# Optimization experiments

Hardware: AMD Instinct MI355X
Metric: run time of the kernel (lower is better)

Reference implementation:

```python
import jax, jax.numpy as jnp
import numpy as np

B, L, D, H, DK, DV = 2, 2048, 1024, 16, 64, 64


def setup_inputs() -> dict:
    key = jax.random.key(0)
    ks = jax.random.split(key, 9)
    s = 0.02
    q = jax.random.normal(ks[0], (B, L, D), dtype=jnp.float32)
    k = jax.random.normal(ks[1], (B, L, D), dtype=jnp.float32)
    v = jax.random.normal(ks[2], (B, L, D), dtype=jnp.float32)
    # causal mask: mask==0 positions are masked out (matches masked_fill(mask==0, -1e9))
    mask = jnp.broadcast_to(jnp.tril(jnp.ones((L, L), dtype=jnp.int32)), (B, L, L))
    Wq = jax.random.normal(ks[3], (D, H * DK), dtype=jnp.float32) * s
    Wk = jax.random.normal(ks[4], (D, H * DK), dtype=jnp.float32) * s
    Wv = jax.random.normal(ks[5], (D, H * DV), dtype=jnp.float32) * s
    Wfc = jax.random.normal(ks[6], (H * DV, D), dtype=jnp.float32) * s
    gamma = jnp.ones((D,), dtype=jnp.float32)
    beta = jnp.zeros((D,), dtype=jnp.float32)
    return {"q": q, "k": k, "v": v, "Wq": Wq, "Wk": Wk, "Wv": Wv,
            "Wfc": Wfc, "gamma": gamma, "beta": beta, "mask": mask}


def reference(q, k, v, Wq, Wk, Wv, Wfc, gamma, beta, mask):
    residual = q
    # project and split heads: [B, H, L, dk]
    qh = (q @ Wq).reshape(B, L, H, DK).transpose(0, 2, 1, 3)
    kh = (k @ Wk).reshape(B, L, H, DK).transpose(0, 2, 1, 3)
    vh = (v @ Wv).reshape(B, L, H, DV).transpose(0, 2, 1, 3)
    temperature = jnp.asarray(DK, jnp.float32) ** 0.5
    scores = jnp.einsum('bhqd,bhkd->bhqk', qh / temperature, kh)  # [B,H,L,L]
    scores = jnp.where(mask[:, None, :, :] == 0, jnp.float32(-1e9), scores)
    attn = jax.nn.softmax(scores, axis=-1)  # dropout = identity (eval)
    out = jnp.einsum('bhqk,bhkd->bhqd', attn, vh)
    out = out.transpose(0, 2, 1, 3).reshape(B, L, H * DV)
    out = out @ Wfc + residual  # dropout = identity (eval)
    # LayerNorm, eps=1e-6
    mu = jnp.mean(out, axis=-1, keepdims=True)
    var = jnp.mean((out - mu) ** 2, axis=-1, keepdims=True)
    out = (out - mu) * jax.lax.rsqrt(var + 1e-6) * gamma + beta
    return out, attn
```

## Files before the change

kernel.cpp:

```cpp
#include <hip/hip_runtime.h>
#include <hip/hip_bf16.h>

#define NB 2
#define NL 2048
#define ND 1024
#define NH 16
#define NDK 64

typedef float fx4 __attribute__((ext_vector_type(4)));
typedef short sx8 __attribute__((ext_vector_type(8)));
typedef short sx4 __attribute__((ext_vector_type(4)));

static __device__ __forceinline__ short f2bf(float x) {
  __hip_bfloat16 h = __float2bfloat16(x);
  short s;
  __builtin_memcpy(&s, &h, 2);
  return s;
}

static __device__ __forceinline__ float ex2(float x) {
  float r; asm("v_exp_f32 %0, %1" : "=v"(r) : "v"(x)); return r;
}

__global__ __launch_bounds__(256) void wt_kernel(
    const float* __restrict__ Wq, const float* __restrict__ Wk,
    const float* __restrict__ Wv, const float* __restrict__ Wfc,
    short* __restrict__ wt)
{
  const float* W = (blockIdx.z==0)?Wq:(blockIdx.z==1)?Wk:(blockIdx.z==2)?Wv:Wfc;
  float sc = (blockIdx.z==0) ? 0.18033688011112042f : 1.0f;
  short* out = wt + (size_t)blockIdx.z*1024*1024;
  int n0 = blockIdx.x*64, k0 = blockIdx.y*64;
  __shared__ float t[64][65];
  int tid = threadIdx.x;
  int kr = tid>>2, ns = (tid&3)*16;
  #pragma unroll
  for (int i=0;i<4;i++){
    fx4 v = *(const fx4*)(W + (size_t)(k0+kr)*1024 + n0 + ns + i*4);
    t[kr][ns+i*4+0]=v[0]; t[kr][ns+i*4+1]=v[1];
    t[kr][ns+i*4+2]=v[2]; t[kr][ns+i*4+3]=v[3];
  }
  __syncthreads();
  int nr = tid>>2, ks = (tid&3)*16;
  sx8 o0,o1;
  #pragma unroll
  for (int i=0;i<8;i++){ o0[i]=f2bf(t[ks+i][nr]*sc); o1[i]=f2bf(t[ks+8+i][nr]*sc); }
  *(sx8*)(out + (size_t)(n0+nr)*1024 + k0 + ks)     = o0;
  *(sx8*)(out + (size_t)(n0+nr)*1024 + k0 + ks + 8) = o1;
}

__global__ __launch_bounds__(256) void cast_kernel(
    const float* __restrict__ q, const float* __restrict__ k,
    const float* __restrict__ v, short* __restrict__ qb,
    short* __restrict__ kb, short* __restrict__ vb)
{
  const float* src = (blockIdx.y==0)?q:(blockIdx.y==1)?k:v;
  short* dst = (blockIdx.y==0)?qb:(blockIdx.y==1)?kb:vb;
  size_t base = ((size_t)blockIdx.x*256 + threadIdx.x)*8;
  fx4 a = *(const fx4*)(src+base), b = *(const fx4*)(src+base+4);
  sx8 o;
  o[0]=f2bf(a[0]); o[1]=f2bf(a[1]); o[2]=f2bf(a[2]); o[3]=f2bf(a[3]);
  o[4]=f2bf(b[0]); o[5]=f2bf(b[1]); o[6]=f2bf(b[2]); o[7]=f2bf(b[3]);
  *(sx8*)(dst+base) = o;
}

__global__ __launch_bounds__(256) void gemm_kernel(
    const short* __restrict__ qb, const short* __restrict__ kb,
    const short* __restrict__ vb, const short* __restrict__ ao,
    const float* __restrict__ q, const short* __restrict__ wt,
    short* __restrict__ qh, short* __restrict__ kh, short* __restrict__ vtb,
    float* __restrict__ preln, int mode_base)
{
  int mode = mode_base + blockIdx.z;
  const short* Ab = (mode==0)?qb:(mode==1)?kb:(mode==2)?vb:ao;
  const short* Bw = wt + (size_t)mode*1048576;
  int m0 = blockIdx.y*128, n0 = blockIdx.x*128;
  __shared__ short Al[128*64];
  __shared__ short Bl[128*64];
  int tid = threadIdx.x;
  int w = tid>>6, l = tid&63, lr = l>>4, lc = l&15;
  int wm = w>>1, wn = w&1;
  int grow = l>>3, gcol = (l&7)*8;

  fx4 acc[4][4];
  #pragma unroll
  for (int i=0;i<4;i++)
    #pragma unroll
    for (int j=0;j<4;j++) acc[i][j] = (fx4)0.0f;

  for (int kb2=0; kb2<1024; kb2+=64) {
    #pragma unroll
    for (int p=0;p<4;p++){
      int rb = w*32 + p*8;
      __builtin_amdgcn_global_load_lds(
        (const __attribute__((address_space(1))) int*)(Ab + (size_t)(m0+rb+grow)*1024 + kb2 + gcol),
        (__attribute__((address_space(3))) int*)&Al[rb*64], 16, 0, 0);
      __builtin_amdgcn_global_load_lds(
        (const __attribute__((address_space(1))) int*)(Bw + (size_t)(n0+rb+grow)*1024 + kb2 + gcol),
        (__attribute__((address_space(3))) int*)&Bl[rb*64], 16, 0, 0);
    }
    __syncthreads();
    #pragma unroll
    for (int kk=0;kk<2;kk++){
      sx8 af[4], bfr[4];
      int oct = kk*4 + lr;
      #pragma unroll
      for (int i=0;i<4;i++){
        af[i]  = *(const sx8*)&Al[(wm*64 + i*16 + lc)*64 + oct*8];
        bfr[i] = *(const sx8*)&Bl[(wn*64 + i*16 + lc)*64 + oct*8];
      }
      #pragma unroll
      for (int i=0;i<4;i++)
        #pragma unroll
        for (int j=0;j<4;j++)
          acc[i][j] = __builtin_amdgcn_mfma_f32_16x16x32_bf16(af[i], bfr[j], acc[i][j], 0,0,0);
    }
    __syncthreads();
  }

  #pragma unroll
  for (int i=0;i<4;i++){
    int mrow0 = m0 + wm*64 + i*16 + lr*4;
    #pragma unroll
    for (int j=0;j<4;j++){
      int n = n0 + wn*64 + j*16 + lc;
      if (mode<=1) {
        short* dst = (mode==0)?qh:kh;
        int hh = n>>6, d = n&63;
        #pragma unroll
        for (int r=0;r<4;r++){
          int mr = mrow0 + r; int bb = mr>>11, lp = mr&2047;
          dst[((size_t)(bb*16+hh)*2048 + lp)*64 + d] = f2bf(acc[i][j][r]);
        }
      } else if (mode==2) {
        int hh = n>>6, d = n&63;
        int bb = mrow0>>11, lp = mrow0&2047;
        sx4 pv;
        #pragma unroll
        for (int r=0;r<4;r++) pv[r] = f2bf(acc[i][j][r]);
        *(sx4*)&vtb[((size_t)(bb*16+hh)*64 + d)*2048 + lp] = pv;
      } else {
        #pragma unroll
        for (int r=0;r<4;r++){
          int mr = mrow0 + r;
          preln[(size_t)mr*1024 + n] = acc[i][j][r] + q[(size_t)mr*1024 + n];
        }
      }
    }
  }
}

__global__ __launch_bounds__(256) void attn_kernel(
    const short* __restrict__ qh, const short* __restrict__ kh,
    const short* __restrict__ vt, short* __restrict__ ao,
    float* __restrict__ attn)
{
  int qt = 31 - (int)blockIdx.x;
  int bh = blockIdx.y;
  int qbase = qt*64;
  int tid = threadIdx.x, w = tid>>6, l = tid&63, lr = l>>4, lc = l&15;
  int qrow0 = qbase + w*16;
  int qrow_l = qrow0 + lc;
  int kend = qrow0 + 16;
  int knlim = (w + 2) & ~1;

  float* arow = attn + (size_t)bh*NL*NL;
  const short* qhb = qh + (size_t)bh*NL*64;
  const short* khb = kh + (size_t)bh*NL*64;
  const short* vtb = vt + (size_t)bh*64*NL;

  sx8 Qf0 = *(const sx8*)&qhb[(size_t)qrow_l*64 + lr*8];
  sx8 Qf1 = *(const sx8*)&qhb[(size_t)qrow_l*64 + 32 + lr*8];

  __shared__ short Kl[2][64][64];
  __shared__ short Vl[2][64][64];
  __shared__ short pl[4][16][40];

  int idx0 = w*64 + l;
  int idx1 = 256 + w*64 + l;
  int rA = idx0>>3, oA = idx0&7, rB = idx1>>3, oB = idx1&7;
  int ntile = qt + 1;

  {
    sx8 ka = *(const sx8*)&khb[(size_t)rA*64 + oA*8];
    sx8 kb = *(const sx8*)&khb[(size_t)rB*64 + oB*8];
    *(sx8*)&Kl[0][rA][(oA^(rA&7))*8] = ka;
    *(sx8*)&Kl[0][rB][(oB^(rB&7))*8] = kb;
  }
  __syncthreads();

  float ls = 0.0f;
  int buf = 0;
  #pragma unroll 1
  for (int t=0; t<ntile; t++){
    bool have_next = (t+1) < ntile;
    sx8 ka, kb;
    if (have_next){
      int nb = (t+1)*64;
      ka = *(const sx8*)&khb[(size_t)(nb+rA)*64 + oA*8];
      kb = *(const sx8*)&khb[(size_t)(nb+rB)*64 + oB*8];
    }
    bool diag = (t == qt);
    #pragma unroll
    for (int kn=0; kn<4; kn++){
      if (diag && kn > w) continue;
      int rk = kn*16 + lc;
      sx8 k0 = *(const sx8*)&Kl[buf][rk][((lr  ^(rk&7))*8)];
      sx8 k1 = *(const sx8*)&Kl[buf][rk][(((lr+4)^(rk&7))*8)];
      fx4 s = (fx4)0.0f;
      s = __builtin_amdgcn_mfma_f32_16x16x32_bf16(k0, Qf0, s, 0,0,0);
      s = __builtin_amdgcn_mfma_f32_16x16x32_bf16(k1, Qf1, s, 0,0,0);
      if (!diag || kn < w) {
        ls += (ex2(s[0]) + ex2(s[1])) + (ex2(s[2]) + ex2(s[3]));
      } else {
        int key0 = t*64 + kn*16 + lr*4;
        #pragma unroll
        for (int r=0;r<4;r++)
          ls += (key0 + r <= qrow_l) ? ex2(s[r]) : 0.0f;
      }
    }
    if (have_next){
      int nbuf = buf ^ 1;
      *(sx8*)&Kl[nbuf][rA][(oA^(rA&7))*8] = ka;
      *(sx8*)&Kl[nbuf][rB][(oB^(rB&7))*8] = kb;
    }
    __syncthreads();
    buf ^= 1;
  }
  ls += __shfl_xor(ls, 16, 64);
  ls += __shfl_xor(ls, 32, 64);
  float inv = 1.0f / ls;

  {
    int fs = ((kend + 31) >> 5) << 5;
    fx4 z = (fx4)0.0f;
    #pragma unroll 1
    for (int r=0; r<16; r++){
      float* rp = &arow[(size_t)(qrow0+r)*NL];
      for (int c = fs + l*4; c < NL; c += 256)
        __builtin_nontemporal_store(z, (fx4*)&rp[c]);
    }
  }

  {
    sx8 ka = *(const sx8*)&khb[(size_t)rA*64 + oA*8];
    sx8 kb = *(const sx8*)&khb[(size_t)rB*64 + oB*8];
    sx8 va = *(const sx8*)&vtb[(size_t)rA*NL + oA*8];
    sx8 vb = *(const sx8*)&vtb[(size_t)rB*NL + oB*8];
    *(sx8*)&Kl[0][rA][(oA^(rA&7))*8] = ka;
    *(sx8*)&Kl[0][rB][(oB^(rB&7))*8] = kb;
    *(sx8*)&Vl[0][rA][(oA^(rA&7))*8] = va;
    *(sx8*)&Vl[0][rB][(oB^(rB&7))*8] = vb;
  }
  __syncthreads();

  fx4 O[4];
  #pragma unroll
  for (int n=0;n<4;n++) O[n] = (fx4)0.0f;

  buf = 0;
  #pragma unroll 1
  for (int t=0; t<ntile; t++){
    int tb = t*64;
    bool have_next = (t+1) < ntile;
    sx8 ka, kb, va, vb;
    if (have_next){
      int nb = tb + 64;
      ka = *(const sx8*)&khb[(size_t)(nb+rA)*64 + oA*8];
      kb = *(const sx8*)&khb[(size_t)(nb+rB)*64 + oB*8];
      va = *(const sx8*)&vtb[(size_t)rA*NL + nb + oA*8];
      vb = *(const sx8*)&vtb[(size_t)rB*NL + nb + oB*8];
    }
    bool diag = (t == qt);
    #pragma unroll
    for (int kn=0; kn<4; kn++){
      fx4 p;
      if (!diag || kn <= w) {
        int rk = kn*16 + lc;
        sx8 k0 = *(const sx8*)&Kl[buf][rk][((lr  ^(rk&7))*8)];
        sx8 k1 = *(const sx8*)&Kl[buf][rk][(((lr+4)^(rk&7))*8)];
        fx4 s = (fx4)0.0f;
        s = __builtin_amdgcn_mfma_f32_16x16x32_bf16(k0, Qf0, s, 0,0,0);
        s = __builtin_amdgcn_mfma_f32_16x16x32_bf16(k1, Qf1, s, 0,0,0);
        if (!diag || kn < w) {
          #pragma unroll
          for (int r=0;r<4;r++) p[r] = ex2(s[r]) * inv;
        } else {
          int key0 = tb + kn*16 + lr*4;
          #pragma unroll
          for (int r=0;r<4;r++)
            p[r] = (key0 + r <= qrow_l) ? ex2(s[r]) * inv : 0.0f;
        }
      } else {
        p = (fx4)0.0f;
      }
      if (!diag || kn < knlim)
        __builtin_nontemporal_store(p, (fx4*)&arow[(size_t)qrow_l*NL + tb + kn*16 + lr*4]);
      sx4 pbv;
      #pragma unroll
      for (int r=0;r<4;r++) pbv[r] = f2bf(p[r]);
      *(sx4*)&pl[w][lc][(kn&1)*16 + lr*4] = pbv;
      if (kn & 1){
        sx8 pf = *(const sx8*)&pl[w][lc][lr*8];
        int t2 = kn>>1;
        #pragma unroll
        for (int n=0;n<4;n++){
          int rv = n*16 + lc;
          sx8 vf = *(const sx8*)&Vl[buf][rv][(((t2*4+lr)^(rv&7))*8)];
          O[n] = __builtin_amdgcn_mfma_f32_16x16x32_bf16(pf, vf, O[n], 0,0,0);
        }
      }
    }
    if (have_next){
      int nbuf = buf ^ 1;
      *(sx8*)&Kl[nbuf][rA][(oA^(rA&7))*8] = ka;
      *(sx8*)&Kl[nbuf][rB][(oB^(rB&7))*8] = kb;
      *(sx8*)&Vl[nbuf][rA][(oA^(rA&7))*8] = va;
      *(sx8*)&Vl[nbuf][rB][(oB^(rB&7))*8] = vb;
    }
    __syncthreads();
    buf ^= 1;
  }

  int bb = bh>>4, hh = bh&15;
  #pragma unroll
  for (int n=0;n<4;n++)
    #pragma unroll
    for (int r=0;r<4;r++)
      ao[((size_t)bb*NL + qrow0 + lr*4 + r)*1024 + hh*64 + n*16 + lc] = f2bf(O[n][r]);
}

__global__ __launch_bounds__(256) void ln_kernel(
    const float* __restrict__ preln, const float* __restrict__ gamma,
    const float* __restrict__ beta, float* __restrict__ out)
{
  int row = blockIdx.x, tid = threadIdx.x;
  fx4 x = *(const fx4*)&preln[(size_t)row*1024 + tid*4];
  float s  = x[0]+x[1]+x[2]+x[3];
  float sq = x[0]*x[0]+x[1]*x[1]+x[2]*x[2]+x[3]*x[3];
  #pragma unroll
  for (int off=1; off<64; off<<=1){
    s  += __shfl_xor(s,  off, 64);
    sq += __shfl_xor(sq, off, 64);
  }
  __shared__ float rs[4], rq[4];
  int w = tid>>6, l = tid&63;
  if (l==0){ rs[w]=s; rq[w]=sq; }
  __syncthreads();
  s  = rs[0]+rs[1]+rs[2]+rs[3];
  sq = rq[0]+rq[1]+rq[2]+rq[3];
  float mean = s*(1.0f/1024.0f);
  float var  = sq*(1.0f/1024.0f) - mean*mean;
  float rstd = rsqrtf(var + 1e-6f);
  fx4 g = *(const fx4*)&gamma[tid*4];
  fx4 b = *(const fx4*)&beta[tid*4];
  fx4 y;
  #pragma unroll
  for (int i=0;i<4;i++) y[i] = (x[i]-mean)*rstd*g[i] + b[i];
  *(fx4*)&out[(size_t)row*1024 + tid*4] = y;
}

extern "C" void kernel_launch(void* const* d_in, const int* in_sizes, int n_in,
                              void* d_out, int out_size, void* d_ws, size_t ws_size,
                              hipStream_t stream) {
  const float* q    = (const float*)d_in[0];
  const float* k    = (const float*)d_in[1];
  const float* v    = (const float*)d_in[2];
  const float* Wq   = (const float*)d_in[3];
  const float* Wk   = (const float*)d_in[4];
  const float* Wv   = (const float*)d_in[5];
  const float* Wfc  = (const float*)d_in[6];
  const float* gamma= (const float*)d_in[7];
  const float* beta = (const float*)d_in[8];

  float* out  = (float*)d_out;
  float* attn = out + (size_t)NB*NL*ND;

  char* ws = (char*)d_ws;
  short* wt    = (short*)(ws);
  short* qb    = (short*)(ws + ((size_t) 8<<20));
  short* kb    = (short*)(ws + ((size_t)16<<20));
  short* vb    = (short*)(ws + ((size_t)24<<20));
  short* qh    = (short*)(ws + ((size_t)32<<20));
  short* kh    = (short*)(ws + ((size_t)40<<20));
  short* vtb   = (short*)(ws + ((size_t)48<<20));
  short* ao    = (short*)(ws + ((size_t)56<<20));
  float* preln = (float*)(ws + ((size_t) 8<<20));

  wt_kernel<<<dim3(16,16,4), 256, 0, stream>>>(Wq, Wk, Wv, Wfc, wt);
  cast_kernel<<<dim3(2048,3), 256, 0, stream>>>(q, k, v, qb, kb, vb);
  gemm_kernel<<<dim3(8,32,3), 256, 0, stream>>>(qb,kb,vb,ao, q, wt, qh,kh,vtb, preln, 0);
  attn_kernel<<<dim3(32,32), 256, 0, stream>>>(qh, kh, vtb, ao, attn);
  gemm_kernel<<<dim3(8,32,1), 256, 0, stream>>>(qb,kb,vb,ao, q, wt, qh,kh,vtb, preln, 3);
  ln_kernel<<<4096, 256, 0, stream>>>(preln, gamma, beta, out);
}
```

Before: 284.1 us.

## Load K/V fragments directly from global into registers, dropping LDS staging and barriers

The attention kernel stops staging K and V tiles through double-buffered shared memory with block-wide barriers. Each wave now loads its MFMA operand fragments straight from global memory into registers, ping-ponging between two register sets for prefetch. This removes the LDS writes and reads and the __syncthreads per tile. In exchange, every wave loads the same K/V data separately (four times the global/L2 traffic), uses more registers, and issues V loads inside the tile without prefetch.

```diff
diff --git a/kernel.cpp b/kernel.cpp
--- a/kernel.cpp
+++ b/kernel.cpp
@@ -163,6 +163,7 @@
   int qrow_l = qrow0 + lc;
   int kend = qrow0 + 16;
   int knlim = (w + 2) & ~1;
+  int ntile = qt + 1;
 
   float* arow = attn + (size_t)bh*NL*NL;
   const short* qhb = qh + (size_t)bh*NL*64;
@@ -172,64 +173,101 @@
   sx8 Qf0 = *(const sx8*)&qhb[(size_t)qrow_l*64 + lr*8];
   sx8 Qf1 = *(const sx8*)&qhb[(size_t)qrow_l*64 + 32 + lr*8];
 
-  __shared__ short Kl[2][64][64];
-  __shared__ short Vl[2][64][64];
   __shared__ short pl[4][16][40];
 
-  int idx0 = w*64 + l;
-  int idx1 = 256 + w*64 + l;
-  int rA = idx0>>3, oA = idx0&7, rB = idx1>>3, oB = idx1&7;
-  int ntile = qt + 1;
-
-  {
-    sx8 ka = *(const sx8*)&khb[(size_t)rA*64 + oA*8];
-    sx8 kb = *(const sx8*)&khb[(size_t)rB*64 + oB*8];
-    *(sx8*)&Kl[0][rA][(oA^(rA&7))*8] = ka;
-    *(sx8*)&Kl[0][rB][(oB^(rB&7))*8] = kb;
-  }
-  __syncthreads();
-
   float ls = 0.0f;
-  int buf = 0;
+  float inv = 0.0f;
+  fx4 O[4];
+  #pragma unroll
+  for (int n=0;n<4;n++) O[n] = (fx4)0.0f;
+
+  auto loadK = [&](sx8 (&Kd)[8], int t){
+    int tb = t*64;
+    #pragma unroll
+    for (int kn=0;kn<4;kn++){
+      Kd[kn*2+0] = *(const sx8*)&khb[(size_t)(tb+kn*16+lc)*64 + lr*8];
+      Kd[kn*2+1] = *(const sx8*)&khb[(size_t)(tb+kn*16+lc)*64 + 32 + lr*8];
+    }
+  };
+
+  auto sumTile = [&](sx8 (&K)[8], int t){
+    bool diag = (t==qt);
+    int tb = t*64;
+    #pragma unroll
+    for (int kn=0;kn<4;kn++){
+      if (diag && kn>w) continue;
+      fx4 s = (fx4)0.0f;
+      s = __builtin_amdgcn_mfma_f32_16x16x32_bf16(K[kn*2+0], Qf0, s, 0,0,0);
+      s = __builtin_amdgcn_mfma_f32_16x16x32_bf16(K[kn*2+1], Qf1, s, 0,0,0);
+      if (!diag || kn<w){
+        ls += (ex2(s[0])+ex2(s[1])) + (ex2(s[2])+ex2(s[3]));
+      } else {
+        int key0 = tb + kn*16 + lr*4;
+        #pragma unroll
+        for (int r=0;r<4;r++)
+          ls += (key0+r <= qrow_l) ? ex2(s[r]) : 0.0f;
+      }
+    }
+  };
+
+  auto pvTile = [&](sx8 (&K)[8], int t){
+    int tb = t*64;
+    bool diag = (t==qt);
+    sx8 Vv[8];
+    #pragma unroll
+    for (int t2=0;t2<2;t2++)
+      #pragma unroll
+      for (int n=0;n<4;n++)
+        Vv[t2*4+n] = *(const sx8*)&vtb[(size_t)(n*16+lc)*NL + tb + t2*32 + lr*8];
+    #pragma unroll
+    for (int kn=0;kn<4;kn++){
+      fx4 p;
+      if (!diag || kn<=w){
+        fx4 s = (fx4)0.0f;
+        s = __builtin_amdgcn_mfma_f32_16x16x32_bf16(K[kn*2+0], Qf0, s, 0,0,0);
+        s = __builtin_amdgcn_mfma_f32_16x16x32_bf16(K[kn*2+1], Qf1, s, 0,0,0);
+        if (!diag || kn<w){
+          #pragma unroll
+          for (int r=0;r<4;r++) p[r] = ex2(s[r]) * inv;
+        } else {
+          int key0 = tb + kn*16 + lr*4;
+          #pragma unroll
+          for (int r=0;r<4;r++)
+            p[r] = (key0+r <= qrow_l) ? ex2(s[r]) * inv : 0.0f;
+        }
+      } else {
+        p = (fx4)0.0f;
+      }
+      if (!diag || kn < knlim)
+        __builtin_nontemporal_store(p, (fx4*)&arow[(size_t)qrow_l*NL + tb + kn*16 + lr*4]);
+      sx4 pbv;
+      #pragma unroll
+      for (int r=0;r<4;r++) pbv[r] = f2bf(p[r]);
+      *(sx4*)&pl[w][lc][(kn&1)*16 + lr*4] = pbv;
+      if (kn & 1){
+        sx8 pf = *(const sx8*)&pl[w][lc][lr*8];
+        #pragma unroll
+        for (int n=0;n<4;n++)
+          O[n] = __builtin_amdgcn_mfma_f32_16x16x32_bf16(pf, Vv[(kn>>1)*4+n], O[n], 0,0,0);
+      }
+    }
+  };
+
+  sx8 kA[8], kB[8];
+
+  loadK(kA, 0);
   #pragma unroll 1
-  for (int t=0; t<ntile; t++){
-    bool have_next = (t+1) < ntile;
-    sx8 ka, kb;
-    if (have_next){
-      int nb = (t+1)*64;
-      ka = *(const sx8*)&khb[(size_t)(nb+rA)*64 + oA*8];
-      kb = *(const sx8*)&khb[(size_t)(nb+rB)*64 + oB*8];
-    }
-    bool diag = (t == qt);
-    #pragma unroll
-    for (int kn=0; kn<4; kn++){
-      if (diag && kn > w) continue;
-      int rk = kn*16 + lc;
-      sx8 k0 = *(const sx8*)&Kl[buf][rk][((lr  ^(rk&7))*8)];
-      sx8 k1 = *(const sx8*)&Kl[buf][rk][(((lr+4)^(rk&7))*8)];
-      fx4 s = (fx4)0.0f;
-      s = __builtin_amdgcn_mfma_f32_16x16x32_bf16(k0, Qf0, s, 0,0,0);
-      s = __builtin_amdgcn_mfma_f32_16x16x32_bf16(k1, Qf1, s, 0,0,0);
-      if (!diag || kn < w) {
-        ls += (ex2(s[0]) + ex2(s[1])) + (ex2(s[2]) + ex2(s[3]));
-      } else {
-        int key0 = t*64 + kn*16 + lr*4;
-        #pragma unroll
-        for (int r=0;r<4;r++)
-          ls += (key0 + r <= qrow_l) ? ex2(s[r]) : 0.0f;
-      }
-    }
-    if (have_next){
-      int nbuf = buf ^ 1;
-      *(sx8*)&Kl[nbuf][rA][(oA^(rA&7))*8] = ka;
-      *(sx8*)&Kl[nbuf][rB][(oB^(rB&7))*8] = kb;
-    }
-    __syncthreads();
-    buf ^= 1;
+  for (int t=0; t<ntile; t+=2){
+    if (t+1<ntile) loadK(kB, t+1);
+    sumTile(kA, t);
+    if (t+1<ntile){
+      if (t+2<ntile) loadK(kA, t+2);
+      sumTile(kB, t+1);
+    }
   }
   ls += __shfl_xor(ls, 16, 64);
   ls += __shfl_xor(ls, 32, 64);
-  float inv = 1.0f / ls;
+  inv = 1.0f / ls;
 
   {
     int fs = ((kend + 31) >> 5) << 5;
@@ -242,84 +280,15 @@
     }
   }
 
-  {
-    sx8 ka = *(const sx8*)&khb[(size_t)rA*64 + oA*8];
-    sx8 kb = *(const sx8*)&khb[(size_t)rB*64 + oB*8];
-    sx8 va = *(const sx8*)&vtb[(size_t)rA*NL + oA*8];
-    sx8 vb = *(const sx8*)&vtb[(size_t)rB*NL + oB*8];
-    *(sx8*)&Kl[0][rA][(oA^(rA&7))*8] = ka;
-    *(sx8*)&Kl[0][rB][(oB^(rB&7))*8] = kb;
-    *(sx8*)&Vl[0][rA][(oA^(rA&7))*8] = va;
-    *(sx8*)&Vl[0][rB][(oB^(rB&7))*8] = vb;
-  }
-  __syncthreads();
-
-  fx4 O[4];
-  #pragma unroll
-  for (int n=0;n<4;n++) O[n] = (fx4)0.0f;
-
-  buf = 0;
+  loadK(kA, 0);
   #pragma unroll 1
-  for (int t=0; t<ntile; t++){
-    int tb = t*64;
-    bool have_next = (t+1) < ntile;
-    sx8 ka, kb, va, vb;
-    if (have_next){
-      int nb = tb + 64;
-      ka = *(const sx8*)&khb[(size_t)(nb+rA)*64 + oA*8];
-      kb = *(const sx8*)&khb[(size_t)(nb+rB)*64 + oB*8];
-      va = *(const sx8*)&vtb[(size_t)rA*NL + nb + oA*8];
-      vb = *(const sx8*)&vtb[(size_t)rB*NL + nb + oB*8];
-    }
-    bool diag = (t == qt);
-    #pragma unroll
-    for (int kn=0; kn<4; kn++){
-      fx4 p;
-      if (!diag || kn <= w) {
-        int rk = kn*16 + lc;
-        sx8 k0 = *(const sx8*)&Kl[buf][rk][((lr  ^(rk&7))*8)];
-        sx8 k1 = *(const sx8*)&Kl[buf][rk][(((lr+4)^(rk&7))*8)];
-        fx4 s = (fx4)0.0f;
-        s = __builtin_amdgcn_mfma_f32_16x16x32_bf16(k0, Qf0, s, 0,0,0);
-        s = __builtin_amdgcn_mfma_f32_16x16x32_bf16(k1, Qf1, s, 0,0,0);
-        if (!diag || kn < w) {
-          #pragma unroll
-          for (int r=0;r<4;r++) p[r] = ex2(s[r]) * inv;
-        } else {
-          int key0 = tb + kn*16 + lr*4;
-          #pragma unroll
-          for (int r=0;r<4;r++)
-            p[r] = (key0 + r <= qrow_l) ? ex2(s[r]) * inv : 0.0f;
-        }
-      } else {
-        p = (fx4)0.0f;
-      }
-      if (!diag || kn < knlim)
-        __builtin_nontemporal_store(p, (fx4*)&arow[(size_t)qrow_l*NL + tb + kn*16 + lr*4]);
-      sx4 pbv;
-      #pragma unroll
-      for (int r=0;r<4;r++) pbv[r] = f2bf(p[r]);
-      *(sx4*)&pl[w][lc][(kn&1)*16 + lr*4] = pbv;
-      if (kn & 1){
-        sx8 pf = *(const sx8*)&pl[w][lc][lr*8];
-        int t2 = kn>>1;
-        #pragma unroll
-        for (int n=0;n<4;n++){
-          int rv = n*16 + lc;
-          sx8 vf = *(const sx8*)&Vl[buf][rv][(((t2*4+lr)^(rv&7))*8)];
-          O[n] = __builtin_amdgcn_mfma_f32_16x16x32_bf16(pf, vf, O[n], 0,0,0);
-        }
-      }
-    }
-    if (have_next){
-      int nbuf = buf ^ 1;
-      *(sx8*)&Kl[nbuf][rA][(oA^(rA&7))*8] = ka;
-      *(sx8*)&Kl[nbuf][rB][(oB^(rB&7))*8] = kb;
-      *(sx8*)&Vl[nbuf][rA][(oA^(rA&7))*8] = va;
-      *(sx8*)&Vl[nbuf][rB][(oB^(rB&7))*8] = vb;
-    }
-    __syncthreads();
-    buf ^= 1;
+  for (int t=0; t<ntile; t+=2){
+    if (t+1<ntile) loadK(kB, t+1);
+    pvTile(kA, t);
+    if (t+1<ntile){
+      if (t+2<ntile) loadK(kA, t+2);
+      pvTile(kB, t+1);
+    }
   }
 
   int bb = bh>>4, hh = bh&15;
```

Result: slower. 457.8 us (+61.1%).
